# Performance work log

Hardware: AMD Instinct MI355X
Metric: run time of the kernel (lower is better)

Reference implementation:

```python
import jax, jax.numpy as jnp
import numpy as np

DIM = 256
NUM_HEADS = 8
HEAD_DIM = DIM // NUM_HEADS
SCALE = 1.0 / DIM ** 0.5  # NOTE: source scales by 1/sqrt(dim), not 1/sqrt(head_dim)


def setup_inputs() -> dict:
    key = jax.random.key(0)
    k_x, k_wqkv, k_wout = jax.random.split(key, 3)
    x = jax.random.normal(k_x, (4, 2048, DIM), dtype=jnp.float32)
    # xavier_uniform for Linear(dim, 3*dim): limit = sqrt(6/(fan_in+fan_out))
    lim_qkv = float(np.sqrt(6.0 / (DIM + 3 * DIM)))
    w_qkv = jax.random.uniform(k_wqkv, (3 * DIM, DIM), minval=-lim_qkv, maxval=lim_qkv, dtype=jnp.float32)
    b_qkv = jnp.zeros((3 * DIM,), dtype=jnp.float32)
    lim_out = float(np.sqrt(6.0 / (DIM + DIM)))
    w_out = jax.random.uniform(k_wout, (DIM, DIM), minval=-lim_out, maxval=lim_out, dtype=jnp.float32)
    b_out = jnp.zeros((DIM,), dtype=jnp.float32)
    return {"x": x, "w_qkv": w_qkv, "b_qkv": b_qkv, "w_out": w_out, "b_out": b_out}


def reference(x, w_qkv, b_qkv, w_out, b_out):
    B, N, C = x.shape
    H, D = NUM_HEADS, C // NUM_HEADS
    qkv = x @ w_qkv.T + b_qkv                       # [B, N, 3C]
    qkv = qkv.reshape(B, N, 3, H, D)
    q = qkv[:, :, 0].transpose(0, 2, 1, 3)          # [B, H, N, D]
    k = qkv[:, :, 1].transpose(0, 2, 1, 3)
    v = qkv[:, :, 2].transpose(0, 2, 1, 3)
    attn = jnp.einsum("bhnd,bhmd->bhnm", q, k) * SCALE  # [B, H, N, N]
    attn = jax.nn.softmax(attn, axis=-1)
    z = jnp.einsum("bhnm,bhmd->bhnd", attn, v)      # [B, H, N, D]
    z = z.transpose(0, 2, 1, 3).reshape(B, N, C)
    return z @ w_out.T + b_out
```

## Files before the change

kernel.cpp:

```cpp
#include <hip/hip_runtime.h>


#define SEQ 2048
#define BATCH 4
#define NHEADS 8
#define HDIM 32
#define DIMC 256
#define SCALE_LOG2E 0.09016844005556021f

typedef __attribute__((ext_vector_type(8))) short short8;
typedef __attribute__((ext_vector_type(4))) float f32x4;

union BF8 { unsigned u[4]; short8 s8; };

__device__ __forceinline__ unsigned pk2bf(float a, float b) {
    union { float f; unsigned u; } ua, ub;
    ua.f = a; ub.f = b;
    return __builtin_amdgcn_perm(ub.u + 0x8000u, ua.u + 0x8000u, 0x07060302u);
}
__device__ __forceinline__ short f2bf(float a) {
    union { float f; unsigned u; } x; x.f = a;
    return (short)((x.u + 0x8000u) >> 16);
}

#define NX (BATCH * SEQ * DIMC)
#define NQW (3 * DIMC * DIMC)
#define NOW (DIMC * DIMC)

__global__ __launch_bounds__(256) void cvt_bf16(const float* __restrict__ x,
                                                const float* __restrict__ wq,
                                                const float* __restrict__ wo,
                                                short* __restrict__ xb,
                                                short* __restrict__ wqb,
                                                short* __restrict__ wob) {
    int i = (blockIdx.x * 256 + threadIdx.x) * 4;
    const float* src;
    short* dst;
    int off;
    if (i < NX) { src = x; dst = xb; off = i; }
    else if (i < NX + NQW) { src = wq; dst = wqb; off = i - NX; }
    else { src = wo; dst = wob; off = i - NX - NQW; }
    float4 v = *(const float4*)&src[off];
    uint2 p;
    p.x = pk2bf(v.x, v.y);
    p.y = pk2bf(v.z, v.w);
    *(uint2*)&dst[off] = p;
}

__global__ __launch_bounds__(256) void qkv_mfma(const short* __restrict__ Xb,
                                                const short* __restrict__ Wb,
                                                const float* __restrict__ bias,
                                                short* __restrict__ Q,
                                                short* __restrict__ Kd,
                                                short* __restrict__ V) {
    __shared__ __align__(16) union SM {
        struct { short A[128][72]; short B[128][72]; } ab;
        short C[128][136];
    } sm;
    const int m0 = blockIdx.y * 128, bx = blockIdx.x;
    const int tid = threadIdx.x;
    const int w = tid >> 6, lane = tid & 63;
    const int m = lane & 15, g = lane >> 4;
    const int wr = w >> 1, wc = w & 1;
    const int srow = tid >> 1, scol = (tid & 1) * 32;

    f32x4 acc[4][4] = {};

    for (int kt = 0; kt < DIMC; kt += 64) {
        short8 a8[4], b8[4];
#pragma unroll
        for (int i = 0; i < 4; i++) {
            a8[i] = *(const short8*)&Xb[(size_t)(m0 + srow) * DIMC + kt + scol + i * 8];
            b8[i] = *(const short8*)&Wb[(size_t)(bx * 128 + srow) * DIMC + kt + scol + i * 8];
        }
        __syncthreads();
#pragma unroll
        for (int i = 0; i < 4; i++) {
            *(short8*)&sm.ab.A[srow][scol + i * 8] = a8[i];
            *(short8*)&sm.ab.B[srow][scol + i * 8] = b8[i];
        }
        __syncthreads();
#pragma unroll
        for (int kk = 0; kk < 2; kk++) {
            short8 af[4], bf[4];
#pragma unroll
            for (int mt = 0; mt < 4; mt++) af[mt] = *(const short8*)&sm.ab.A[wr * 64 + mt * 16 + m][kk * 32 + g * 8];
#pragma unroll
            for (int nt = 0; nt < 4; nt++) bf[nt] = *(const short8*)&sm.ab.B[wc * 64 + nt * 16 + m][kk * 32 + g * 8];
#pragma unroll
            for (int mt = 0; mt < 4; mt++)
#pragma unroll
                for (int nt = 0; nt < 4; nt++)
                    acc[mt][nt] = __builtin_amdgcn_mfma_f32_16x16x32_bf16(af[mt], bf[nt], acc[mt][nt], 0, 0, 0);
        }
    }

    const int which = bx >> 1;
    const int h0 = (bx & 1) * 4;
    const int bidx = blockIdx.y >> 4;
    const int ntok0 = (blockIdx.y & 15) * 128;
    float bv[4];
#pragma unroll
    for (int nt = 0; nt < 4; nt++) bv[nt] = bias[bx * 128 + wc * 64 + nt * 16 + m];

    __syncthreads();
    if (which != 2) {
        const float qs = (which == 0) ? SCALE_LOG2E : 1.0f;
#pragma unroll
        for (int mt = 0; mt < 4; mt++)
#pragma unroll
            for (int nt = 0; nt < 4; nt++)
#pragma unroll
                for (int r = 0; r < 4; r++)
                    sm.C[wr * 64 + mt * 16 + g * 4 + r][wc * 64 + nt * 16 + m] =
                        f2bf((acc[mt][nt][r] + bv[nt]) * qs);
        __syncthreads();
        short* dst = (which == 0) ? Q : Kd;
        const int tok = tid >> 1, d0 = (tid & 1) * 16;
#pragma unroll
        for (int hh = 0; hh < 4; hh++) {
            size_t o = ((size_t)((bidx * NHEADS + h0 + hh) * SEQ) + ntok0 + tok) * HDIM + d0;
            *(short8*)&dst[o] = *(const short8*)&sm.C[tok][hh * 32 + d0];
            *(short8*)&dst[o + 8] = *(const short8*)&sm.C[tok][hh * 32 + d0 + 8];
        }
    } else {
#pragma unroll
        for (int mt = 0; mt < 4; mt++)
#pragma unroll
            for (int nt = 0; nt < 4; nt++) {
                uint2 p;
                p.x = pk2bf(acc[mt][nt][0] + bv[nt], acc[mt][nt][1] + bv[nt]);
                p.y = pk2bf(acc[mt][nt][2] + bv[nt], acc[mt][nt][3] + bv[nt]);
                *(uint2*)&sm.C[wc * 64 + nt * 16 + m][wr * 64 + mt * 16 + g * 4] = p;
            }
        __syncthreads();
        const int col = tid >> 1, t0 = (tid & 1) * 64;
        const int hh = col >> 5, d = col & 31;
        size_t o = ((size_t)((bidx * NHEADS + h0 + hh) * HDIM) + d) * SEQ + ntok0 + t0;
#pragma unroll
        for (int c2 = 0; c2 < 8; c2++)
            *(short8*)&V[o + c2 * 8] = *(const short8*)&sm.C[col][t0 + c2 * 8];
    }
}

__global__ __launch_bounds__(256) void attn_stream(const short* __restrict__ Q,
                                                   const short* __restrict__ K,
                                                   const short* __restrict__ V,
                                                   short* __restrict__ Zb) {
    const int bh = blockIdx.y;
    const int b = bh >> 3, h = bh & 7;
    const int q0 = blockIdx.x * 128;
    const short* qb = Q + (size_t)bh * SEQ * HDIM;
    const short* kb = K + (size_t)bh * SEQ * HDIM;
    const short* vb = V + (size_t)bh * HDIM * SEQ;
    const int tid = threadIdx.x;
    const int w = tid >> 6, lane = tid & 63;
    const int m = lane & 15, g = lane >> 4;

    short8 qf[2];
    qf[0] = *(const short8*)(qb + (size_t)(q0 + w * 32 + m) * HDIM + g * 8);
    qf[1] = *(const short8*)(qb + (size_t)(q0 + w * 32 + 16 + m) * HDIM + g * 8);

    int koff[4];
#pragma unroll
    for (int t = 0; t < 4; t++) {
        int row = 32 * (t >> 1) + ((m >> 2) << 3) + ((t & 1) << 2) + (m & 3);
        koff[t] = row * HDIM + g * 8;
    }
    const int voff0 = m * SEQ + g * 8;
    const int voff1 = (m + 16) * SEQ + g * 8;

    f32x4 o00 = {0.f, 0.f, 0.f, 0.f}, o01 = {0.f, 0.f, 0.f, 0.f};
    f32x4 o10 = {0.f, 0.f, 0.f, 0.f}, o11 = {0.f, 0.f, 0.f, 0.f};
    f32x4 ol0 = {0.f, 0.f, 0.f, 0.f}, ol1 = {0.f, 0.f, 0.f, 0.f};
    const short8 ones = {0x3F80, 0x3F80, 0x3F80, 0x3F80, 0x3F80, 0x3F80, 0x3F80, 0x3F80};

    for (int k0 = 0; k0 < SEQ; k0 += 64) {
        short8 kf[4];
#pragma unroll
        for (int t = 0; t < 4; t++)
            kf[t] = *(const short8*)(kb + (size_t)k0 * HDIM + koff[t]);
        short8 vf00 = *(const short8*)(vb + voff0 + k0);
        short8 vf01 = *(const short8*)(vb + voff1 + k0);
        short8 vf10 = *(const short8*)(vb + voff0 + k0 + 32);
        short8 vf11 = *(const short8*)(vb + voff1 + k0 + 32);

#pragma unroll
        for (int qh = 0; qh < 2; qh++) {
            f32x4 st[4];
#pragma unroll
            for (int t = 0; t < 4; t++) {
                f32x4 z4 = {0.f, 0.f, 0.f, 0.f};
                st[t] = __builtin_amdgcn_mfma_f32_16x16x32_bf16(kf[t], qh ? qf[1] : qf[0], z4, 0, 0, 0);
            }
            BF8 a0, a1;
#pragma unroll
            for (int t = 0; t < 2; t++) {
                a0.u[t * 2 + 0] = pk2bf(__builtin_amdgcn_exp2f(st[t][0]), __builtin_amdgcn_exp2f(st[t][1]));
                a0.u[t * 2 + 1] = pk2bf(__builtin_amdgcn_exp2f(st[t][2]), __builtin_amdgcn_exp2f(st[t][3]));
                a1.u[t * 2 + 0] = pk2bf(__builtin_amdgcn_exp2f(st[t + 2][0]), __builtin_amdgcn_exp2f(st[t + 2][1]));
                a1.u[t * 2 + 1] = pk2bf(__builtin_amdgcn_exp2f(st[t + 2][2]), __builtin_amdgcn_exp2f(st[t + 2][3]));
            }
            if (qh == 0) {
                o00 = __builtin_amdgcn_mfma_f32_16x16x32_bf16(a0.s8, vf00, o00, 0, 0, 0);
                o01 = __builtin_amdgcn_mfma_f32_16x16x32_bf16(a0.s8, vf01, o01, 0, 0, 0);
                ol0 = __builtin_amdgcn_mfma_f32_16x16x32_bf16(a0.s8, ones, ol0, 0, 0, 0);
                o00 = __builtin_amdgcn_mfma_f32_16x16x32_bf16(a1.s8, vf10, o00, 0, 0, 0);
                o01 = __builtin_amdgcn_mfma_f32_16x16x32_bf16(a1.s8, vf11, o01, 0, 0, 0);
                ol0 = __builtin_amdgcn_mfma_f32_16x16x32_bf16(a1.s8, ones, ol0, 0, 0, 0);
            } else {
                o10 = __builtin_amdgcn_mfma_f32_16x16x32_bf16(a0.s8, vf00, o10, 0, 0, 0);
                o11 = __builtin_amdgcn_mfma_f32_16x16x32_bf16(a0.s8, vf01, o11, 0, 0, 0);
                ol1 = __builtin_amdgcn_mfma_f32_16x16x32_bf16(a0.s8, ones, ol1, 0, 0, 0);
                o10 = __builtin_amdgcn_mfma_f32_16x16x32_bf16(a1.s8, vf10, o10, 0, 0, 0);
                o11 = __builtin_amdgcn_mfma_f32_16x16x32_bf16(a1.s8, vf11, o11, 0, 0, 0);
                ol1 = __builtin_amdgcn_mfma_f32_16x16x32_bf16(a1.s8, ones, ol1, 0, 0, 0);
            }
        }
    }

#pragma unroll
    for (int qh = 0; qh < 2; qh++) {
        f32x4 oa = qh ? o10 : o00;
        f32x4 ob = qh ? o11 : o01;
        f32x4 ll = qh ? ol1 : ol0;
#pragma unroll
        for (int r = 0; r < 4; r++) {
            float inv = __builtin_amdgcn_rcpf(ll[r]);
            int row = q0 + w * 32 + qh * 16 + g * 4 + r;
            size_t zo = ((size_t)(b * SEQ + row)) * DIMC + h * HDIM + m;
            Zb[zo] = f2bf(oa[r] * inv);
            Zb[zo + 16] = f2bf(ob[r] * inv);
        }
    }
}

__global__ __launch_bounds__(256) void out_mfma(const short* __restrict__ A,
                                                const short* __restrict__ Wb,
                                                const float* __restrict__ bias,
                                                float* __restrict__ C) {
    __shared__ __align__(16) short As[128][72];
    __shared__ __align__(16) short Bs[64][72];
    const int m0 = blockIdx.y * 128, n0 = blockIdx.x * 64;
    const int tid = threadIdx.x;
    const int w = tid >> 6, lane = tid & 63;
    const int m = lane & 15, g = lane >> 4;
    const int wr = w >> 1, wc = w & 1;
    const int arow = tid >> 1, acol = (tid & 1) * 32;
    const int brow = tid >> 2, bcol = (tid & 3) * 16;

    f32x4 acc[4][2] = {};

    for (int kt = 0; kt < DIMC; kt += 64) {
        short8 a8[4], b8[2];
#pragma unroll
        for (int i = 0; i < 4; i++)
            a8[i] = *(const short8*)&A[(size_t)(m0 + arow) * DIMC + kt + acol + i * 8];
#pragma unroll
        for (int i = 0; i < 2; i++)
            b8[i] = *(const short8*)&Wb[(size_t)(n0 + brow) * DIMC + kt + bcol + i * 8];
        __syncthreads();
#pragma unroll
        for (int i = 0; i < 4; i++) *(short8*)&As[arow][acol + i * 8] = a8[i];
#pragma unroll
        for (int i = 0; i < 2; i++) *(short8*)&Bs[brow][bcol + i * 8] = b8[i];
        __syncthreads();
#pragma unroll
        for (int kk = 0; kk < 2; kk++) {
            short8 af[4], bf2[2];
#pragma unroll
            for (int mt = 0; mt < 4; mt++) af[mt] = *(const short8*)&As[wr * 64 + mt * 16 + m][kk * 32 + g * 8];
#pragma unroll
            for (int nt = 0; nt < 2; nt++) bf2[nt] = *(const short8*)&Bs[wc * 32 + nt * 16 + m][kk * 32 + g * 8];
#pragma unroll
            for (int mt = 0; mt < 4; mt++)
#pragma unroll
                for (int nt = 0; nt < 2; nt++)
                    acc[mt][nt] = __builtin_amdgcn_mfma_f32_16x16x32_bf16(af[mt], bf2[nt], acc[mt][nt], 0, 0, 0);
        }
    }

    float bv[2];
    bv[0] = bias[n0 + wc * 32 + m];
    bv[1] = bias[n0 + wc * 32 + 16 + m];
#pragma unroll
    for (int mt = 0; mt < 4; mt++)
#pragma unroll
        for (int nt = 0; nt < 2; nt++)
#pragma unroll
            for (int r = 0; r < 4; r++)
                C[(size_t)(m0 + wr * 64 + mt * 16 + g * 4 + r) * DIMC + n0 + wc * 32 + nt * 16 + m] =
                    acc[mt][nt][r] + bv[nt];
}

extern "C" void kernel_launch(void* const* d_in, const int* in_sizes, int n_in,
                              void* d_out, int out_size, void* d_ws, size_t ws_size,
                              hipStream_t stream) {
    const float* x     = (const float*)d_in[0];
    const float* w_qkv = (const float*)d_in[1];
    const float* b_qkv = (const float*)d_in[2];
    const float* w_out = (const float*)d_in[3];
    const float* b_out = (const float*)d_in[4];
    float* out = (float*)d_out;

    const size_t HSZ = (size_t)BATCH * NHEADS * SEQ * HDIM;
    short* xb  = (short*)d_ws;
    short* wqb = xb + NX;
    short* wob = wqb + NQW;
    short* qw  = wob + NOW;
    short* kw  = qw + HSZ;
    short* vw  = kw + HSZ;
    short* zb  = vw + HSZ;

    cvt_bf16<<<(NX + NQW + NOW) / 1024, 256, 0, stream>>>(x, w_qkv, w_out, xb, wqb, wob);
    qkv_mfma<<<dim3(6, 64), 256, 0, stream>>>(xb, wqb, b_qkv, qw, kw, vw);
    attn_stream<<<dim3(16, 32), 256, 0, stream>>>(qw, kw, vw, zb);
    out_mfma<<<dim3(4, 64), 256, 0, stream>>>(zb, wob, b_out, out);
}
```

Baseline: 132.5 us.

## Shrink tiles, drop LDS staging in GEMMs, prefetch K/V in attention

The QKV and output projection GEMMs now load MFMA operand fragments straight from global memory rather than staging them through shared memory, and use smaller tiles so twice as many blocks launch. The attention kernel handles 64 query rows per block instead of 128, doubling the grid, and software-prefetches the next K/V tile into registers while the current one is computed. All three kernels get a launch-bounds occupancy hint. The goal is more parallelism and latency hiding on the GPU's many CUs, paid for with less operand reuse per block and more global/L2 traffic.

```diff
diff --git a/kernel.cpp b/kernel.cpp
--- a/kernel.cpp
+++ b/kernel.cpp
@@ -47,109 +47,94 @@
     *(uint2*)&dst[off] = p;
 }
 
-__global__ __launch_bounds__(256) void qkv_mfma(const short* __restrict__ Xb,
-                                                const short* __restrict__ Wb,
-                                                const float* __restrict__ bias,
-                                                short* __restrict__ Q,
-                                                short* __restrict__ Kd,
-                                                short* __restrict__ V) {
-    __shared__ __align__(16) union SM {
-        struct { short A[128][72]; short B[128][72]; } ab;
-        short C[128][136];
-    } sm;
+__global__ __launch_bounds__(256, 4) void qkv_mfma(const short* __restrict__ Xb,
+                                                   const short* __restrict__ Wb,
+                                                   const float* __restrict__ bias,
+                                                   short* __restrict__ Q,
+                                                   short* __restrict__ Kd,
+                                                   short* __restrict__ V) {
+    __shared__ __align__(16) short Cs[128 * 72];
+
     const int m0 = blockIdx.y * 128, bx = blockIdx.x;
     const int tid = threadIdx.x;
     const int w = tid >> 6, lane = tid & 63;
     const int m = lane & 15, g = lane >> 4;
-    const int wr = w >> 1, wc = w & 1;
-    const int srow = tid >> 1, scol = (tid & 1) * 32;
-
-    f32x4 acc[4][4] = {};
-
-    for (int kt = 0; kt < DIMC; kt += 64) {
-        short8 a8[4], b8[4];
-#pragma unroll
-        for (int i = 0; i < 4; i++) {
-            a8[i] = *(const short8*)&Xb[(size_t)(m0 + srow) * DIMC + kt + scol + i * 8];
-            b8[i] = *(const short8*)&Wb[(size_t)(bx * 128 + srow) * DIMC + kt + scol + i * 8];
-        }
-        __syncthreads();
-#pragma unroll
-        for (int i = 0; i < 4; i++) {
-            *(short8*)&sm.ab.A[srow][scol + i * 8] = a8[i];
-            *(short8*)&sm.ab.B[srow][scol + i * 8] = b8[i];
-        }
-        __syncthreads();
-#pragma unroll
-        for (int kk = 0; kk < 2; kk++) {
-            short8 af[4], bf[4];
-#pragma unroll
-            for (int mt = 0; mt < 4; mt++) af[mt] = *(const short8*)&sm.ab.A[wr * 64 + mt * 16 + m][kk * 32 + g * 8];
-#pragma unroll
-            for (int nt = 0; nt < 4; nt++) bf[nt] = *(const short8*)&sm.ab.B[wc * 64 + nt * 16 + m][kk * 32 + g * 8];
-#pragma unroll
-            for (int mt = 0; mt < 4; mt++)
-#pragma unroll
-                for (int nt = 0; nt < 4; nt++)
-                    acc[mt][nt] = __builtin_amdgcn_mfma_f32_16x16x32_bf16(af[mt], bf[nt], acc[mt][nt], 0, 0, 0);
-        }
-    }
-
-    const int which = bx >> 1;
-    const int h0 = (bx & 1) * 4;
+
+    f32x4 acc[2][4] = {};
+
+    const short* arow0 = Xb + (size_t)(m0 + w * 32 + m) * DIMC + g * 8;
+    const short* brow0 = Wb + (size_t)(bx * 64 + m) * DIMC + g * 8;
+
+#pragma unroll 2
+    for (int kt = 0; kt < DIMC; kt += 32) {
+        short8 af[2], bf[4];
+#pragma unroll
+        for (int mt = 0; mt < 2; mt++)
+            af[mt] = *(const short8*)(arow0 + mt * 16 * DIMC + kt);
+#pragma unroll
+        for (int nt = 0; nt < 4; nt++)
+            bf[nt] = *(const short8*)(brow0 + nt * 16 * DIMC + kt);
+#pragma unroll
+        for (int mt = 0; mt < 2; mt++)
+#pragma unroll
+            for (int nt = 0; nt < 4; nt++)
+                acc[mt][nt] = __builtin_amdgcn_mfma_f32_16x16x32_bf16(af[mt], bf[nt], acc[mt][nt], 0, 0, 0);
+    }
+
+    const int which = bx >> 2;
+    const int h0 = (bx & 3) * 2;
     const int bidx = blockIdx.y >> 4;
     const int ntok0 = (blockIdx.y & 15) * 128;
     float bv[4];
 #pragma unroll
-    for (int nt = 0; nt < 4; nt++) bv[nt] = bias[bx * 128 + wc * 64 + nt * 16 + m];
-
-    __syncthreads();
+    for (int nt = 0; nt < 4; nt++) bv[nt] = bias[bx * 64 + nt * 16 + m];
+
     if (which != 2) {
         const float qs = (which == 0) ? SCALE_LOG2E : 1.0f;
 #pragma unroll
-        for (int mt = 0; mt < 4; mt++)
+        for (int mt = 0; mt < 2; mt++)
 #pragma unroll
             for (int nt = 0; nt < 4; nt++)
 #pragma unroll
                 for (int r = 0; r < 4; r++)
-                    sm.C[wr * 64 + mt * 16 + g * 4 + r][wc * 64 + nt * 16 + m] =
+                    Cs[(w * 32 + mt * 16 + g * 4 + r) * 72 + nt * 16 + m] =
                         f2bf((acc[mt][nt][r] + bv[nt]) * qs);
         __syncthreads();
         short* dst = (which == 0) ? Q : Kd;
         const int tok = tid >> 1, d0 = (tid & 1) * 16;
 #pragma unroll
-        for (int hh = 0; hh < 4; hh++) {
+        for (int hh = 0; hh < 2; hh++) {
             size_t o = ((size_t)((bidx * NHEADS + h0 + hh) * SEQ) + ntok0 + tok) * HDIM + d0;
-            *(short8*)&dst[o] = *(const short8*)&sm.C[tok][hh * 32 + d0];
-            *(short8*)&dst[o + 8] = *(const short8*)&sm.C[tok][hh * 32 + d0 + 8];
+            *(short8*)&dst[o] = *(const short8*)&Cs[tok * 72 + hh * 32 + d0];
+            *(short8*)&dst[o + 8] = *(const short8*)&Cs[tok * 72 + hh * 32 + d0 + 8];
         }
     } else {
 #pragma unroll
-        for (int mt = 0; mt < 4; mt++)
+        for (int mt = 0; mt < 2; mt++)
 #pragma unroll
             for (int nt = 0; nt < 4; nt++) {
                 uint2 p;
                 p.x = pk2bf(acc[mt][nt][0] + bv[nt], acc[mt][nt][1] + bv[nt]);
                 p.y = pk2bf(acc[mt][nt][2] + bv[nt], acc[mt][nt][3] + bv[nt]);
-                *(uint2*)&sm.C[wc * 64 + nt * 16 + m][wr * 64 + mt * 16 + g * 4] = p;
+                *(uint2*)&Cs[(nt * 16 + m) * 136 + w * 32 + mt * 16 + g * 4] = p;
             }
         __syncthreads();
-        const int col = tid >> 1, t0 = (tid & 1) * 64;
+        const int col = tid >> 2, t0 = (tid & 3) * 32;
         const int hh = col >> 5, d = col & 31;
         size_t o = ((size_t)((bidx * NHEADS + h0 + hh) * HDIM) + d) * SEQ + ntok0 + t0;
 #pragma unroll
-        for (int c2 = 0; c2 < 8; c2++)
-            *(short8*)&V[o + c2 * 8] = *(const short8*)&sm.C[col][t0 + c2 * 8];
-    }
-}
-
-__global__ __launch_bounds__(256) void attn_stream(const short* __restrict__ Q,
-                                                   const short* __restrict__ K,
-                                                   const short* __restrict__ V,
-                                                   short* __restrict__ Zb) {
+        for (int c2 = 0; c2 < 4; c2++)
+            *(short8*)&V[o + c2 * 8] = *(const short8*)&Cs[col * 136 + t0 + c2 * 8];
+    }
+}
+
+__global__ __launch_bounds__(256, 4) void attn_stream(const short* __restrict__ Q,
+                                                      const short* __restrict__ K,
+                                                      const short* __restrict__ V,
+                                                      short* __restrict__ Zb) {
     const int bh = blockIdx.y;
     const int b = bh >> 3, h = bh & 7;
-    const int q0 = blockIdx.x * 128;
+    const int q0 = blockIdx.x * 64;
     const short* qb = Q + (size_t)bh * SEQ * HDIM;
     const short* kb = K + (size_t)bh * SEQ * HDIM;
     const short* vb = V + (size_t)bh * HDIM * SEQ;
@@ -157,9 +142,7 @@
     const int w = tid >> 6, lane = tid & 63;
     const int m = lane & 15, g = lane >> 4;
 
-    short8 qf[2];
-    qf[0] = *(const short8*)(qb + (size_t)(q0 + w * 32 + m) * HDIM + g * 8);
-    qf[1] = *(const short8*)(qb + (size_t)(q0 + w * 32 + 16 + m) * HDIM + g * 8);
+    const short8 qf = *(const short8*)(qb + (size_t)(q0 + w * 16 + m) * HDIM + g * 8);
 
     int koff[4];
 #pragma unroll
@@ -170,127 +153,101 @@
     const int voff0 = m * SEQ + g * 8;
     const int voff1 = (m + 16) * SEQ + g * 8;
 
-    f32x4 o00 = {0.f, 0.f, 0.f, 0.f}, o01 = {0.f, 0.f, 0.f, 0.f};
-    f32x4 o10 = {0.f, 0.f, 0.f, 0.f}, o11 = {0.f, 0.f, 0.f, 0.f};
-    f32x4 ol0 = {0.f, 0.f, 0.f, 0.f}, ol1 = {0.f, 0.f, 0.f, 0.f};
+    f32x4 o0 = {0.f, 0.f, 0.f, 0.f};
+    f32x4 o1 = {0.f, 0.f, 0.f, 0.f};
+    f32x4 ol = {0.f, 0.f, 0.f, 0.f};
     const short8 ones = {0x3F80, 0x3F80, 0x3F80, 0x3F80, 0x3F80, 0x3F80, 0x3F80, 0x3F80};
 
+    short8 kf[4], vf[4];
+#pragma unroll
+    for (int t = 0; t < 4; t++) kf[t] = *(const short8*)(kb + koff[t]);
+    vf[0] = *(const short8*)(vb + voff0);
+    vf[1] = *(const short8*)(vb + voff1);
+    vf[2] = *(const short8*)(vb + voff0 + 32);
+    vf[3] = *(const short8*)(vb + voff1 + 32);
+
     for (int k0 = 0; k0 < SEQ; k0 += 64) {
-        short8 kf[4];
+        const int kn = (k0 + 64 < SEQ) ? k0 + 64 : 0;
+        short8 kfn[4], vfn[4];
 #pragma unroll
         for (int t = 0; t < 4; t++)
-            kf[t] = *(const short8*)(kb + (size_t)k0 * HDIM + koff[t]);
-        short8 vf00 = *(const short8*)(vb + voff0 + k0);
-        short8 vf01 = *(const short8*)(vb + voff1 + k0);
-        short8 vf10 = *(const short8*)(vb + voff0 + k0 + 32);
-        short8 vf11 = *(const short8*)(vb + voff1 + k0 + 32);
-
-#pragma unroll
-        for (int qh = 0; qh < 2; qh++) {
-            f32x4 st[4];
-#pragma unroll
-            for (int t = 0; t < 4; t++) {
-                f32x4 z4 = {0.f, 0.f, 0.f, 0.f};
-                st[t] = __builtin_amdgcn_mfma_f32_16x16x32_bf16(kf[t], qh ? qf[1] : qf[0], z4, 0, 0, 0);
-            }
-            BF8 a0, a1;
-#pragma unroll
-            for (int t = 0; t < 2; t++) {
-                a0.u[t * 2 + 0] = pk2bf(__builtin_amdgcn_exp2f(st[t][0]), __builtin_amdgcn_exp2f(st[t][1]));
-                a0.u[t * 2 + 1] = pk2bf(__builtin_amdgcn_exp2f(st[t][2]), __builtin_amdgcn_exp2f(st[t][3]));
-                a1.u[t * 2 + 0] = pk2bf(__builtin_amdgcn_exp2f(st[t + 2][0]), __builtin_amdgcn_exp2f(st[t + 2][1]));
-                a1.u[t * 2 + 1] = pk2bf(__builtin_amdgcn_exp2f(st[t + 2][2]), __builtin_amdgcn_exp2f(st[t + 2][3]));
-            }
-            if (qh == 0) {
-                o00 = __builtin_amdgcn_mfma_f32_16x16x32_bf16(a0.s8, vf00, o00, 0, 0, 0);
-                o01 = __builtin_amdgcn_mfma_f32_16x16x32_bf16(a0.s8, vf01, o01, 0, 0, 0);
-                ol0 = __builtin_amdgcn_mfma_f32_16x16x32_bf16(a0.s8, ones, ol0, 0, 0, 0);
-                o00 = __builtin_amdgcn_mfma_f32_16x16x32_bf16(a1.s8, vf10, o00, 0, 0, 0);
-                o01 = __builtin_amdgcn_mfma_f32_16x16x32_bf16(a1.s8, vf11, o01, 0, 0, 0);
-                ol0 = __builtin_amdgcn_mfma_f32_16x16x32_bf16(a1.s8, ones, ol0, 0, 0, 0);
-            } else {
-                o10 = __builtin_amdgcn_mfma_f32_16x16x32_bf16(a0.s8, vf00, o10, 0, 0, 0);
-                o11 = __builtin_amdgcn_mfma_f32_16x16x32_bf16(a0.s8, vf01, o11, 0, 0, 0);
-                ol1 = __builtin_amdgcn_mfma_f32_16x16x32_bf16(a0.s8, ones, ol1, 0, 0, 0);
-                o10 = __builtin_amdgcn_mfma_f32_16x16x32_bf16(a1.s8, vf10, o10, 0, 0, 0);
-                o11 = __builtin_amdgcn_mfma_f32_16x16x32_bf16(a1.s8, vf11, o11, 0, 0, 0);
-                ol1 = __builtin_amdgcn_mfma_f32_16x16x32_bf16(a1.s8, ones, ol1, 0, 0, 0);
-            }
+            kfn[t] = *(const short8*)(kb + (size_t)kn * HDIM + koff[t]);
+        vfn[0] = *(const short8*)(vb + voff0 + kn);
+        vfn[1] = *(const short8*)(vb + voff1 + kn);
+        vfn[2] = *(const short8*)(vb + voff0 + kn + 32);
+        vfn[3] = *(const short8*)(vb + voff1 + kn + 32);
+
+        f32x4 st[4];
+#pragma unroll
+        for (int t = 0; t < 4; t++) {
+            f32x4 z4 = {0.f, 0.f, 0.f, 0.f};
+            st[t] = __builtin_amdgcn_mfma_f32_16x16x32_bf16(kf[t], qf, z4, 0, 0, 0);
         }
-    }
-
-#pragma unroll
-    for (int qh = 0; qh < 2; qh++) {
-        f32x4 oa = qh ? o10 : o00;
-        f32x4 ob = qh ? o11 : o01;
-        f32x4 ll = qh ? ol1 : ol0;
-#pragma unroll
-        for (int r = 0; r < 4; r++) {
-            float inv = __builtin_amdgcn_rcpf(ll[r]);
-            int row = q0 + w * 32 + qh * 16 + g * 4 + r;
-            size_t zo = ((size_t)(b * SEQ + row)) * DIMC + h * HDIM + m;
-            Zb[zo] = f2bf(oa[r] * inv);
-            Zb[zo + 16] = f2bf(ob[r] * inv);
-        }
-    }
-}
-
-__global__ __launch_bounds__(256) void out_mfma(const short* __restrict__ A,
-                                                const short* __restrict__ Wb,
-                                                const float* __restrict__ bias,
-                                                float* __restrict__ C) {
-    __shared__ __align__(16) short As[128][72];
-    __shared__ __align__(16) short Bs[64][72];
-    const int m0 = blockIdx.y * 128, n0 = blockIdx.x * 64;
+
+        BF8 a0, a1;
+        a0.u[0] = pk2bf(__builtin_amdgcn_exp2f(st[0][0]), __builtin_amdgcn_exp2f(st[0][1]));
+        a0.u[1] = pk2bf(__builtin_amdgcn_exp2f(st[0][2]), __builtin_amdgcn_exp2f(st[0][3]));
+        a0.u[2] = pk2bf(__builtin_amdgcn_exp2f(st[1][0]), __builtin_amdgcn_exp2f(st[1][1]));
+        a0.u[3] = pk2bf(__builtin_amdgcn_exp2f(st[1][2]), __builtin_amdgcn_exp2f(st[1][3]));
+        a1.u[0] = pk2bf(__builtin_amdgcn_exp2f(st[2][0]), __builtin_amdgcn_exp2f(st[2][1]));
+        a1.u[1] = pk2bf(__builtin_amdgcn_exp2f(st[2][2]), __builtin_amdgcn_exp2f(st[2][3]));
+        a1.u[2] = pk2bf(__builtin_amdgcn_exp2f(st[3][0]), __builtin_amdgcn_exp2f(st[3][1]));
+        a1.u[3] = pk2bf(__builtin_amdgcn_exp2f(st[3][2]), __builtin_amdgcn_exp2f(st[3][3]));
+
+        o0 = __builtin_amdgcn_mfma_f32_16x16x32_bf16(a0.s8, vf[0], o0, 0, 0, 0);
+        o1 = __builtin_amdgcn_mfma_f32_16x16x32_bf16(a0.s8, vf[1], o1, 0, 0, 0);
+        ol = __builtin_amdgcn_mfma_f32_16x16x32_bf16(a0.s8, ones, ol, 0, 0, 0);
+        o0 = __builtin_amdgcn_mfma_f32_16x16x32_bf16(a1.s8, vf[2], o0, 0, 0, 0);
+        o1 = __builtin_amdgcn_mfma_f32_16x16x32_bf16(a1.s8, vf[3], o1, 0, 0, 0);
+        ol = __builtin_amdgcn_mfma_f32_16x16x32_bf16(a1.s8, ones, ol, 0, 0, 0);
+
+#pragma unroll
+        for (int t = 0; t < 4; t++) { kf[t] = kfn[t]; vf[t] = vfn[t]; }
+    }
+
+#pragma unroll
+    for (int r = 0; r < 4; r++) {
+        float inv = __builtin_amdgcn_rcpf(ol[r]);
+        int row = q0 + w * 16 + g * 4 + r;
+        size_t zo = ((size_t)(b * SEQ + row)) * DIMC + h * HDIM + m;
+        Zb[zo] = f2bf(o0[r] * inv);
+        Zb[zo + 16] = f2bf(o1[r] * inv);
+    }
+}
+
+__global__ __launch_bounds__(256, 4) void out_mfma(const short* __restrict__ A,
+                                                   const short* __restrict__ Wb,
+                                                   const float* __restrict__ bias,
+                                                   float* __restrict__ C) {
+    const int m0 = blockIdx.y * 64, n0 = blockIdx.x * 64;
     const int tid = threadIdx.x;
     const int w = tid >> 6, lane = tid & 63;
     const int m = lane & 15, g = lane >> 4;
-    const int wr = w >> 1, wc = w & 1;
-    const int arow = tid >> 1, acol = (tid & 1) * 32;
-    const int brow = tid >> 2, bcol = (tid & 3) * 16;
-
-    f32x4 acc[4][2] = {};
-
-    for (int kt = 0; kt < DIMC; kt += 64) {
-        short8 a8[4], b8[2];
-#pragma unroll
-        for (int i = 0; i < 4; i++)
-            a8[i] = *(const short8*)&A[(size_t)(m0 + arow) * DIMC + kt + acol + i * 8];
-#pragma unroll
-        for (int i = 0; i < 2; i++)
-            b8[i] = *(const short8*)&Wb[(size_t)(n0 + brow) * DIMC + kt + bcol + i * 8];
-        __syncthreads();
-#pragma unroll
-        for (int i = 0; i < 4; i++) *(short8*)&As[arow][acol + i * 8] = a8[i];
-#pragma unroll
-        for (int i = 0; i < 2; i++) *(short8*)&Bs[brow][bcol + i * 8] = b8[i];
-        __syncthreads();
-#pragma unroll
-        for (int kk = 0; kk < 2; kk++) {
-            short8 af[4], bf2[2];
-#pragma unroll
-            for (int mt = 0; mt < 4; mt++) af[mt] = *(const short8*)&As[wr * 64 + mt * 16 + m][kk * 32 + g * 8];
-#pragma unroll
-            for (int nt = 0; nt < 2; nt++) bf2[nt] = *(const short8*)&Bs[wc * 32 + nt * 16 + m][kk * 32 + g * 8];
-#pragma unroll
-            for (int mt = 0; mt < 4; mt++)
-#pragma unroll
-                for (int nt = 0; nt < 2; nt++)
-                    acc[mt][nt] = __builtin_amdgcn_mfma_f32_16x16x32_bf16(af[mt], bf2[nt], acc[mt][nt], 0, 0, 0);
-        }
-    }
-
-    float bv[2];
-    bv[0] = bias[n0 + wc * 32 + m];
-    bv[1] = bias[n0 + wc * 32 + 16 + m];
-#pragma unroll
-    for (int mt = 0; mt < 4; mt++)
-#pragma unroll
-        for (int nt = 0; nt < 2; nt++)
-#pragma unroll
-            for (int r = 0; r < 4; r++)
-                C[(size_t)(m0 + wr * 64 + mt * 16 + g * 4 + r) * DIMC + n0 + wc * 32 + nt * 16 + m] =
-                    acc[mt][nt][r] + bv[nt];
+
+    f32x4 acc[4] = {};
+    const short* arow = A + (size_t)(m0 + w * 16 + m) * DIMC + g * 8;
+    const short* brow = Wb + (size_t)(n0 + m) * DIMC + g * 8;
+
+#pragma unroll 2
+    for (int kt = 0; kt < DIMC; kt += 32) {
+        short8 af = *(const short8*)(arow + kt);
+        short8 bf[4];
+#pragma unroll
+        for (int nt = 0; nt < 4; nt++)
+            bf[nt] = *(const short8*)(brow + nt * 16 * DIMC + kt);
+#pragma unroll
+        for (int nt = 0; nt < 4; nt++)
+            acc[nt] = __builtin_amdgcn_mfma_f32_16x16x32_bf16(af, bf[nt], acc[nt], 0, 0, 0);
+    }
+
+    float bv[4];
+#pragma unroll
+    for (int nt = 0; nt < 4; nt++) bv[nt] = bias[n0 + nt * 16 + m];
+#pragma unroll
+    for (int nt = 0; nt < 4; nt++)
+#pragma unroll
+        for (int r = 0; r < 4; r++)
+            C[(size_t)(m0 + w * 16 + g * 4 + r) * DIMC + n0 + nt * 16 + m] = acc[nt][r] + bv[nt];
 }
 
 extern "C" void kernel_launch(void* const* d_in, const int* in_sizes, int n_in,
@@ -313,7 +270,7 @@
     short* zb  = vw + HSZ;
 
     cvt_bf16<<<(NX + NQW + NOW) / 1024, 256, 0, stream>>>(x, w_qkv, w_out, xb, wqb, wob);
-    qkv_mfma<<<dim3(6, 64), 256, 0, stream>>>(xb, wqb, b_qkv, qw, kw, vw);
-    attn_stream<<<dim3(16, 32), 256, 0, stream>>>(qw, kw, vw, zb);
-    out_mfma<<<dim3(4, 64), 256, 0, stream>>>(zb, wob, b_out, out);
-}
+    qkv_mfma<<<dim3(12, 64), 256, 0, stream>>>(xb, wqb, b_qkv, qw, kw, vw);
+    attn_stream<<<dim3(32, 32), 256, 0, stream>>>(qw, kw, vw, zb);
+    out_mfma<<<dim3(4, 128), 256, 0, stream>>>(zb, wob, b_out, out);
+}
```

Result: slower. 187.8 us (+41.8%).

## Restructure attention into LDS-staged KV tiles split across waves

Applied to the files above, without the earlier changes.

The attention kernel now handles 64 queries per block and streams 128-key K/V tiles through double-buffered shared memory, with each wave taking a 32-key slice instead of every wave reading all keys from global memory. Partial outputs and row sums from the four waves are reduced through shared memory in the epilogue, and Z is written as 16-byte vector stores. The grid doubles to 1024 blocks. This targets redundant global/L2 K/V traffic and the poor occupancy of 512 blocks, at the cost of a barrier per tile, extra LDS traffic and a cross-wave reduction.

```diff
diff --git a/kernel.cpp b/kernel.cpp
--- a/kernel.cpp
+++ b/kernel.cpp
@@ -143,13 +143,18 @@
     }
 }
 
-__global__ __launch_bounds__(256) void attn_stream(const short* __restrict__ Q,
-                                                   const short* __restrict__ K,
-                                                   const short* __restrict__ V,
-                                                   short* __restrict__ Zb) {
+__global__ __launch_bounds__(256) void attn_tile(const short* __restrict__ Q,
+                                                 const short* __restrict__ K,
+                                                 const short* __restrict__ V,
+                                                 short* __restrict__ Zb) {
+    __shared__ __align__(16) union SM {
+        struct { short Ks[2][128][40]; short Vs[2][32][136]; } kv;
+        struct { float O[4][64][36]; float L[4][64]; } ep;
+    } sm;
+
     const int bh = blockIdx.y;
     const int b = bh >> 3, h = bh & 7;
-    const int q0 = blockIdx.x * 128;
+    const int q0 = blockIdx.x * 64;
     const short* qb = Q + (size_t)bh * SEQ * HDIM;
     const short* kb = K + (size_t)bh * SEQ * HDIM;
     const short* vb = V + (size_t)bh * HDIM * SEQ;
@@ -157,82 +162,97 @@
     const int w = tid >> 6, lane = tid & 63;
     const int m = lane & 15, g = lane >> 4;
 
-    short8 qf[2];
-    qf[0] = *(const short8*)(qb + (size_t)(q0 + w * 32 + m) * HDIM + g * 8);
-    qf[1] = *(const short8*)(qb + (size_t)(q0 + w * 32 + 16 + m) * HDIM + g * 8);
-
-    int koff[4];
-#pragma unroll
-    for (int t = 0; t < 4; t++) {
-        int row = 32 * (t >> 1) + ((m >> 2) << 3) + ((t & 1) << 2) + (m & 3);
-        koff[t] = row * HDIM + g * 8;
-    }
-    const int voff0 = m * SEQ + g * 8;
-    const int voff1 = (m + 16) * SEQ + g * 8;
-
-    f32x4 o00 = {0.f, 0.f, 0.f, 0.f}, o01 = {0.f, 0.f, 0.f, 0.f};
-    f32x4 o10 = {0.f, 0.f, 0.f, 0.f}, o11 = {0.f, 0.f, 0.f, 0.f};
-    f32x4 ol0 = {0.f, 0.f, 0.f, 0.f}, ol1 = {0.f, 0.f, 0.f, 0.f};
+    short8 qfr[4];
+#pragma unroll
+    for (int qt = 0; qt < 4; qt++)
+        qfr[qt] = *(const short8*)(qb + (size_t)(q0 + qt * 16 + m) * HDIM + g * 8);
+
+    const int krow = tid >> 1, kcol = (tid & 1) * 16;
+    const int rl = krow & 31;
+    const int lrow = (krow & ~31) | (((rl >> 2) & 1) << 4) | ((rl >> 3) << 2) | (rl & 3);
+    const int vrow = tid >> 3, vcol = (tid & 7) * 16;
+
+    f32x4 o[4][2] = {};
+    f32x4 ol[4] = {};
     const short8 ones = {0x3F80, 0x3F80, 0x3F80, 0x3F80, 0x3F80, 0x3F80, 0x3F80, 0x3F80};
 
-    for (int k0 = 0; k0 < SEQ; k0 += 64) {
-        short8 kf[4];
-#pragma unroll
-        for (int t = 0; t < 4; t++)
-            kf[t] = *(const short8*)(kb + (size_t)k0 * HDIM + koff[t]);
-        short8 vf00 = *(const short8*)(vb + voff0 + k0);
-        short8 vf01 = *(const short8*)(vb + voff1 + k0);
-        short8 vf10 = *(const short8*)(vb + voff0 + k0 + 32);
-        short8 vf11 = *(const short8*)(vb + voff1 + k0 + 32);
-
-#pragma unroll
-        for (int qh = 0; qh < 2; qh++) {
-            f32x4 st[4];
-#pragma unroll
-            for (int t = 0; t < 4; t++) {
-                f32x4 z4 = {0.f, 0.f, 0.f, 0.f};
-                st[t] = __builtin_amdgcn_mfma_f32_16x16x32_bf16(kf[t], qh ? qf[1] : qf[0], z4, 0, 0, 0);
-            }
-            BF8 a0, a1;
-#pragma unroll
-            for (int t = 0; t < 2; t++) {
-                a0.u[t * 2 + 0] = pk2bf(__builtin_amdgcn_exp2f(st[t][0]), __builtin_amdgcn_exp2f(st[t][1]));
-                a0.u[t * 2 + 1] = pk2bf(__builtin_amdgcn_exp2f(st[t][2]), __builtin_amdgcn_exp2f(st[t][3]));
-                a1.u[t * 2 + 0] = pk2bf(__builtin_amdgcn_exp2f(st[t + 2][0]), __builtin_amdgcn_exp2f(st[t + 2][1]));
-                a1.u[t * 2 + 1] = pk2bf(__builtin_amdgcn_exp2f(st[t + 2][2]), __builtin_amdgcn_exp2f(st[t + 2][3]));
-            }
-            if (qh == 0) {
-                o00 = __builtin_amdgcn_mfma_f32_16x16x32_bf16(a0.s8, vf00, o00, 0, 0, 0);
-                o01 = __builtin_amdgcn_mfma_f32_16x16x32_bf16(a0.s8, vf01, o01, 0, 0, 0);
-                ol0 = __builtin_amdgcn_mfma_f32_16x16x32_bf16(a0.s8, ones, ol0, 0, 0, 0);
-                o00 = __builtin_amdgcn_mfma_f32_16x16x32_bf16(a1.s8, vf10, o00, 0, 0, 0);
-                o01 = __builtin_amdgcn_mfma_f32_16x16x32_bf16(a1.s8, vf11, o01, 0, 0, 0);
-                ol0 = __builtin_amdgcn_mfma_f32_16x16x32_bf16(a1.s8, ones, ol0, 0, 0, 0);
-            } else {
-                o10 = __builtin_amdgcn_mfma_f32_16x16x32_bf16(a0.s8, vf00, o10, 0, 0, 0);
-                o11 = __builtin_amdgcn_mfma_f32_16x16x32_bf16(a0.s8, vf01, o11, 0, 0, 0);
-                ol1 = __builtin_amdgcn_mfma_f32_16x16x32_bf16(a0.s8, ones, ol1, 0, 0, 0);
-                o10 = __builtin_amdgcn_mfma_f32_16x16x32_bf16(a1.s8, vf10, o10, 0, 0, 0);
-                o11 = __builtin_amdgcn_mfma_f32_16x16x32_bf16(a1.s8, vf11, o11, 0, 0, 0);
-                ol1 = __builtin_amdgcn_mfma_f32_16x16x32_bf16(a1.s8, ones, ol1, 0, 0, 0);
-            }
-        }
-    }
-
-#pragma unroll
-    for (int qh = 0; qh < 2; qh++) {
-        f32x4 oa = qh ? o10 : o00;
-        f32x4 ob = qh ? o11 : o01;
-        f32x4 ll = qh ? ol1 : ol0;
-#pragma unroll
-        for (int r = 0; r < 4; r++) {
-            float inv = __builtin_amdgcn_rcpf(ll[r]);
-            int row = q0 + w * 32 + qh * 16 + g * 4 + r;
-            size_t zo = ((size_t)(b * SEQ + row)) * DIMC + h * HDIM + m;
-            Zb[zo] = f2bf(oa[r] * inv);
-            Zb[zo + 16] = f2bf(ob[r] * inv);
-        }
-    }
+    short8 k0a = *(const short8*)(kb + (size_t)krow * HDIM + kcol);
+    short8 k0b = *(const short8*)(kb + (size_t)krow * HDIM + kcol + 8);
+    short8 v0a = *(const short8*)(vb + (size_t)vrow * SEQ + vcol);
+    short8 v0b = *(const short8*)(vb + (size_t)vrow * SEQ + vcol + 8);
+    *(short8*)&sm.kv.Ks[0][lrow][kcol] = k0a;
+    *(short8*)&sm.kv.Ks[0][lrow][kcol + 8] = k0b;
+    *(short8*)&sm.kv.Vs[0][vrow][vcol] = v0a;
+    *(short8*)&sm.kv.Vs[0][vrow][vcol + 8] = v0b;
+    __syncthreads();
+
+    for (int it = 0; it < SEQ / 128; ++it) {
+        const int buf = it & 1;
+        if (it < SEQ / 128 - 1) {
+            const int kn = (it + 1) * 128;
+            k0a = *(const short8*)(kb + (size_t)(kn + krow) * HDIM + kcol);
+            k0b = *(const short8*)(kb + (size_t)(kn + krow) * HDIM + kcol + 8);
+            v0a = *(const short8*)(vb + (size_t)vrow * SEQ + kn + vcol);
+            v0b = *(const short8*)(vb + (size_t)vrow * SEQ + kn + vcol + 8);
+        }
+
+        short8 kf0 = *(const short8*)&sm.kv.Ks[buf][w * 32 + m][g * 8];
+        short8 kf1 = *(const short8*)&sm.kv.Ks[buf][w * 32 + 16 + m][g * 8];
+        short8 vf0 = *(const short8*)&sm.kv.Vs[buf][m][w * 32 + g * 8];
+        short8 vf1 = *(const short8*)&sm.kv.Vs[buf][16 + m][w * 32 + g * 8];
+
+#pragma unroll
+        for (int qt = 0; qt < 4; qt++) {
+            f32x4 z4 = {0.f, 0.f, 0.f, 0.f};
+            f32x4 st0 = __builtin_amdgcn_mfma_f32_16x16x32_bf16(kf0, qfr[qt], z4, 0, 0, 0);
+            f32x4 st1 = __builtin_amdgcn_mfma_f32_16x16x32_bf16(kf1, qfr[qt], z4, 0, 0, 0);
+            BF8 a;
+            a.u[0] = pk2bf(__builtin_amdgcn_exp2f(st0[0]), __builtin_amdgcn_exp2f(st0[1]));
+            a.u[1] = pk2bf(__builtin_amdgcn_exp2f(st0[2]), __builtin_amdgcn_exp2f(st0[3]));
+            a.u[2] = pk2bf(__builtin_amdgcn_exp2f(st1[0]), __builtin_amdgcn_exp2f(st1[1]));
+            a.u[3] = pk2bf(__builtin_amdgcn_exp2f(st1[2]), __builtin_amdgcn_exp2f(st1[3]));
+            o[qt][0] = __builtin_amdgcn_mfma_f32_16x16x32_bf16(a.s8, vf0, o[qt][0], 0, 0, 0);
+            o[qt][1] = __builtin_amdgcn_mfma_f32_16x16x32_bf16(a.s8, vf1, o[qt][1], 0, 0, 0);
+            ol[qt] = __builtin_amdgcn_mfma_f32_16x16x32_bf16(a.s8, ones, ol[qt], 0, 0, 0);
+        }
+
+        if (it < SEQ / 128 - 1) {
+            const int nb = buf ^ 1;
+            *(short8*)&sm.kv.Ks[nb][lrow][kcol] = k0a;
+            *(short8*)&sm.kv.Ks[nb][lrow][kcol + 8] = k0b;
+            *(short8*)&sm.kv.Vs[nb][vrow][vcol] = v0a;
+            *(short8*)&sm.kv.Vs[nb][vrow][vcol + 8] = v0b;
+        }
+        __syncthreads();
+    }
+
+#pragma unroll
+    for (int qt = 0; qt < 4; qt++) {
+#pragma unroll
+        for (int dh = 0; dh < 2; dh++)
+#pragma unroll
+            for (int r = 0; r < 4; r++)
+                sm.ep.O[w][qt * 16 + g * 4 + r][dh * 16 + m] = o[qt][dh][r];
+        if (m == 0)
+#pragma unroll
+            for (int r = 0; r < 4; r++)
+                sm.ep.L[w][qt * 16 + g * 4 + r] = ol[qt][r];
+    }
+    __syncthreads();
+
+    const int ql = tid >> 2, d0 = (tid & 3) * 8;
+    float lt = sm.ep.L[0][ql] + sm.ep.L[1][ql] + sm.ep.L[2][ql] + sm.ep.L[3][ql];
+    float inv = __builtin_amdgcn_rcpf(lt);
+    float sv[8];
+#pragma unroll
+    for (int j = 0; j < 8; j++)
+        sv[j] = sm.ep.O[0][ql][d0 + j] + sm.ep.O[1][ql][d0 + j] +
+                sm.ep.O[2][ql][d0 + j] + sm.ep.O[3][ql][d0 + j];
+    BF8 pz;
+#pragma unroll
+    for (int j = 0; j < 4; j++)
+        pz.u[j] = pk2bf(sv[2 * j] * inv, sv[2 * j + 1] * inv);
+    *(short8*)&Zb[(size_t)(b * SEQ + q0 + ql) * DIMC + h * HDIM + d0] = pz.s8;
 }
 
 __global__ __launch_bounds__(256) void out_mfma(const short* __restrict__ A,
@@ -314,6 +334,6 @@
 
     cvt_bf16<<<(NX + NQW + NOW) / 1024, 256, 0, stream>>>(x, w_qkv, w_out, xb, wqb, wob);
     qkv_mfma<<<dim3(6, 64), 256, 0, stream>>>(xb, wqb, b_qkv, qw, kw, vw);
-    attn_stream<<<dim3(16, 32), 256, 0, stream>>>(qw, kw, vw, zb);
+    attn_tile<<<dim3(32, 32), 256, 0, stream>>>(qw, kw, vw, zb);
     out_mfma<<<dim3(4, 64), 256, 0, stream>>>(zb, wob, b_out, out);
 }
```

Measured after the change: 122.7 us. -7.4%, faster.
